# Performance work log

Hardware: AMD Instinct MI355X
Metric: run time of the kernel (lower is better)

## Reference

```python
import jax, jax.numpy as jnp
import numpy as np

N_QUBITS = 8
N_LAYERS = 7


def setup_inputs() -> dict:
    key = jax.random.key(0)
    ks = jax.random.split(key, 6)
    B = 65536
    return {
        "x": jax.random.normal(ks[0], (B, 2 ** N_QUBITS), dtype=jnp.float32),
        "weights": jax.random.normal(ks[1], (N_LAYERS, N_QUBITS), dtype=jnp.float32),
        "W1": jax.random.normal(ks[2], (16, 1), dtype=jnp.float32) * 0.5,
        "b1": jax.random.normal(ks[3], (16,), dtype=jnp.float32) * 0.1,
        "W2": jax.random.normal(ks[4], (1, 16), dtype=jnp.float32) * 0.5,
        "b2": jax.random.normal(ks[5], (1,), dtype=jnp.float32) * 0.1,
    }


def _apply_ry(psi, q, theta):
    # RY(theta) = [[cos(t/2), -sin(t/2)], [sin(t/2), cos(t/2)]] on wire q (axis q+1)
    c = jnp.cos(theta * 0.5)
    s = jnp.sin(theta * 0.5)
    a = jnp.take(psi, 0, axis=q + 1)
    b = jnp.take(psi, 1, axis=q + 1)
    return jnp.stack([c * a - s * b, s * a + c * b], axis=q + 1)


def _apply_cnot(psi, q):
    # CNOT control=q, target=q+1: flip target amplitudes where control=1
    ctl0 = jnp.take(psi, 0, axis=q + 1)
    ctl1 = jnp.take(psi, 1, axis=q + 1)
    # after removing axis q+1, target wire q+1 sits at axis q+1 of the slice
    ctl1 = jnp.flip(ctl1, axis=q + 1)
    return jnp.stack([ctl0, ctl1], axis=q + 1)


def _circuit(x, weights):
    B = x.shape[0]
    # AmplitudeEmbedding(normalize=True): real input -> real state (RY, CNOT are real)
    psi = x / jnp.linalg.norm(x, axis=1, keepdims=True)
    psi = psi.reshape((B,) + (2,) * N_QUBITS)  # axis 1 == wire 0 (MSB)
    for l in range(N_LAYERS):
        for q in range(N_QUBITS):
            psi = _apply_ry(psi, q, weights[l, q])
        for q in range(N_QUBITS - 1):
            psi = _apply_cnot(psi, q)
    probs = (psi ** 2).reshape(B, 2, -1)
    # <PauliZ(0)> = P(wire0=0) - P(wire0=1)
    return jnp.sum(probs[:, 0] - probs[:, 1], axis=1)


def reference(x, weights, W1, b1, W2, b2):
    z = _circuit(x, weights)[:, None]          # [B, 1]
    h = jax.nn.relu(z @ W1.T + b1)             # [B, 16]
    return jax.nn.sigmoid(h @ W2.T + b2)       # [B, 1]
```

## Files before the change

### kernel.cpp

```cpp
#include <hip/hip_runtime.h>
#include <hip/hip_bf16.h>

typedef __attribute__((ext_vector_type(8))) short bf16x8;
typedef __attribute__((ext_vector_type(4))) float f32x4;

__device__ __forceinline__ unsigned short f2bf(float f) {
    unsigned u = __builtin_bit_cast(unsigned, f);
    unsigned rnd = 0x7FFFu + ((u >> 16) & 1u);
    return (unsigned short)((u + rnd) >> 16);
}

__device__ __forceinline__ void wg_barrier() {
    asm volatile("s_waitcnt lgkmcnt(0)" ::: "memory");
    __builtin_amdgcn_sched_barrier(0);
    __builtin_amdgcn_s_barrier();
    __builtin_amdgcn_sched_barrier(0);
}

__global__ __launch_bounds__(256) void qnn_setup(const float* __restrict__ wts,
                                                 unsigned short* __restrict__ Bp) {
    __shared__ float cs[56], sn[56];
    int tid = threadIdx.x;
    if (tid < 56) {
        float th = 0.5f * wts[tid];
        cs[tid] = cosf(th);
        sn[tid] = sinf(th);
    }
    __syncthreads();

    int l = tid & 63;
    int k = blockIdx.x * 4 + (tid >> 6);
    int a0 = l << 2;

    float v0 = (float)(a0 + 0 == k);
    float v1 = (float)(a0 + 1 == k);
    float v2 = (float)(a0 + 2 == k);
    float v3 = (float)(a0 + 3 == k);

#pragma unroll
    for (int L = 0; L < 7; ++L) {
#pragma unroll
        for (int q = 0; q <= 5; ++q) {
            int m = 5 - q;
            float c = cs[L * 8 + q], s = sn[L * 8 + q];
            float ss = ((l >> m) & 1) ? s : -s;
            float p0 = __shfl_xor(v0, 1 << m);
            float p1 = __shfl_xor(v1, 1 << m);
            float p2 = __shfl_xor(v2, 1 << m);
            float p3 = __shfl_xor(v3, 1 << m);
            v0 = fmaf(ss, p0, c * v0);
            v1 = fmaf(ss, p1, c * v1);
            v2 = fmaf(ss, p2, c * v2);
            v3 = fmaf(ss, p3, c * v3);
        }
        {
            float c = cs[L * 8 + 6], s = sn[L * 8 + 6];
            float n0 = fmaf(-s, v2, c * v0), n2 = fmaf(s, v0, c * v2);
            float n1 = fmaf(-s, v3, c * v1), n3 = fmaf(s, v1, c * v3);
            v0 = n0; v1 = n1; v2 = n2; v3 = n3;
        }
        {
            float c = cs[L * 8 + 7], s = sn[L * 8 + 7];
            float n0 = fmaf(-s, v1, c * v0), n1 = fmaf(s, v0, c * v1);
            float n2 = fmaf(-s, v3, c * v2), n3 = fmaf(s, v2, c * v3);
            v0 = n0; v1 = n1; v2 = n2; v3 = n3;
        }
        {
            int src = l;
#pragma unroll
            for (int q = 4; q >= 0; --q)
                src = src ^ (((src >> (5 - q)) & 1) << (4 - q));
            v0 = __shfl(v0, src);
            v1 = __shfl(v1, src);
            v2 = __shfl(v2, src);
            v3 = __shfl(v3, src);
        }
        {
            bool cc = (l & 1);
            float n0 = cc ? v2 : v0, n2 = cc ? v0 : v2;
            float n1 = cc ? v3 : v1, n3 = cc ? v1 : v3;
            v0 = n0; v1 = n1; v2 = n2; v3 = n3;
        }
        {
            float t = v2; v2 = v3; v3 = t;
        }
    }

    int t = k >> 5, j = k & 7, lk = (k >> 3) & 3;
#pragma unroll
    for (int r = 0; r < 4; ++r) {
        int n = a0 + r;
        int u = n >> 4;
        int ls = lk * 16 + (n & 15);
        float val = (r == 0) ? v0 : (r == 1) ? v1 : (r == 2) ? v2 : v3;
        Bp[(((u * 8 + t) * 64) + ls) * 8 + j] = f2bf(val);
    }
}

__device__ __forceinline__ void cvt_store(const float4& a, const float4& b,
                                          unsigned short (*Xp)[256],
                                          int sr, int qt) {
    bf16x8 h;
    h[0] = (short)f2bf(a.x); h[1] = (short)f2bf(a.y);
    h[2] = (short)f2bf(a.z); h[3] = (short)f2bf(a.w);
    h[4] = (short)f2bf(b.x); h[5] = (short)f2bf(b.y);
    h[6] = (short)f2bf(b.z); h[7] = (short)f2bf(b.w);
    *(bf16x8*)&Xp[sr][(qt ^ (sr & 7)) * 8] = h;
}

__global__ __launch_bounds__(512, 4) void qnn_main(
    const float* __restrict__ x, const unsigned short* __restrict__ Bp,
    const float* __restrict__ W1, const float* __restrict__ b1,
    const float* __restrict__ W2, const float* __restrict__ b2,
    float* __restrict__ out) {
    __shared__ __align__(16) unsigned short Xs[2][16][256];
    __shared__ float Qpart[8][128];

    int tid = threadIdx.x;
    int l = tid & 63, w = tid >> 6;
    int sr = tid >> 5, qt = tid & 31;
    size_t base = (size_t)blockIdx.x * 128 * 256;
    const float* xst = x + base + (size_t)sr * 256 + qt * 8;

    const unsigned short* up = Bp + (size_t)(2 * w) * 4096 + l * 8;
    bf16x8 uf0[8], uf1[8];
#pragma unroll
    for (int t = 0; t < 8; ++t) {
        uf0[t] = *(const bf16x8*)(up + t * 512);
        uf1[t] = *(const bf16x8*)(up + 4096 + t * 512);
    }

    float4 pf[2][2];
    pf[0][0] = *(const float4*)(xst);
    pf[0][1] = *(const float4*)(xst + 4);
    pf[1][0] = *(const float4*)(xst + 4096);
    pf[1][1] = *(const float4*)(xst + 4100);
    cvt_store(pf[0][0], pf[0][1], Xs[0], sr, qt);
    wg_barrier();

    int row = l & 15, kg = l >> 4;

#pragma unroll
    for (int t = 0; t < 8; ++t) {
        if (t + 2 < 8) {
            pf[t & 1][0] = *(const float4*)(xst + (size_t)(t + 2) * 4096);
            pf[t & 1][1] = *(const float4*)(xst + (size_t)(t + 2) * 4096 + 4);
        }
        {
            const unsigned short* rp = &Xs[t & 1][row][0];
            f32x4 a0 = {0.f, 0.f, 0.f, 0.f}, a1 = {0.f, 0.f, 0.f, 0.f};
#pragma unroll
            for (int ks = 0; ks < 8; ++ks) {
                bf16x8 xf = *(const bf16x8*)(rp + (((ks << 2) | kg) ^ (row & 7)) * 8);
                a0 = __builtin_amdgcn_mfma_f32_16x16x32_bf16(uf0[ks], xf, a0, 0, 0, 0);
                a1 = __builtin_amdgcn_mfma_f32_16x16x32_bf16(uf1[ks], xf, a1, 0, 0, 0);
            }
            float q = 0.f;
#pragma unroll
            for (int j = 0; j < 4; ++j)
                q = fmaf(a0[j], a0[j], fmaf(a1[j], a1[j], q));
            q += __shfl_xor(q, 16);
            q += __shfl_xor(q, 32);
            if (l < 16) Qpart[w][t * 16 + l] = q;
        }
        if (t + 1 < 8)
            cvt_store(pf[(t + 1) & 1][0], pf[(t + 1) & 1][1],
                      Xs[(t + 1) & 1], sr, qt);
        wg_barrier();
    }

    if (tid < 128) {
        float pp = Qpart[0][tid] + Qpart[1][tid] + Qpart[2][tid] + Qpart[3][tid];
        float pm = Qpart[4][tid] + Qpart[5][tid] + Qpart[6][tid] + Qpart[7][tid];
        float z = (pp - pm) / (pp + pm);
        float o = b2[0];
#pragma unroll
        for (int jj = 0; jj < 16; ++jj) {
            float h = fmaf(z, W1[jj], b1[jj]);
            h = h > 0.f ? h : 0.f;
            o = fmaf(W2[jj], h, o);
        }
        out[(size_t)blockIdx.x * 128 + tid] = 1.f / (1.f + expf(-o));
    }
}

extern "C" void kernel_launch(void* const* d_in, const int* in_sizes, int n_in,
                              void* d_out, int out_size, void* d_ws, size_t ws_size,
                              hipStream_t stream) {
    const float* x   = (const float*)d_in[0];
    const float* wts = (const float*)d_in[1];
    const float* W1  = (const float*)d_in[2];
    const float* b1  = (const float*)d_in[3];
    const float* W2  = (const float*)d_in[4];
    const float* b2  = (const float*)d_in[5];
    float* out = (float*)d_out;
    unsigned short* Bp = (unsigned short*)d_ws;

    int B = in_sizes[0] >> 8;
    qnn_setup<<<64, 256, 0, stream>>>(wts, Bp);
    qnn_main<<<B / 128, 512, 0, stream>>>(x, Bp, W1, b1, W2, b2, out);
}
```

Baseline: 22.94 us.

## Process 32-row stages with wider per-thread loads and MFMA priority boost

The staged pipeline now handles 32 rows of x per stage instead of 16, halving the number of barrier-separated iterations. Each thread loads 16 floats (four float4) per stage, and each wave runs two 16-row MFMA groups per stage. s_setprio is raised around the MFMA section so compute waves get issue priority over the conversion and store work. The trade-off is double the LDS tile size and more prefetch registers per thread, which may reduce occupancy under the launch bound of 4.

```diff
diff --git a/kernel.cpp b/kernel.cpp
--- a/kernel.cpp
+++ b/kernel.cpp
@@ -97,15 +97,20 @@
     }
 }
 
-__device__ __forceinline__ void cvt_store(const float4& a, const float4& b,
+__device__ __forceinline__ void cvt_store(const float4* pf,
                                           unsigned short (*Xp)[256],
                                           int sr, int qt) {
-    bf16x8 h;
-    h[0] = (short)f2bf(a.x); h[1] = (short)f2bf(a.y);
-    h[2] = (short)f2bf(a.z); h[3] = (short)f2bf(a.w);
-    h[4] = (short)f2bf(b.x); h[5] = (short)f2bf(b.y);
-    h[6] = (short)f2bf(b.z); h[7] = (short)f2bf(b.w);
-    *(bf16x8*)&Xp[sr][(qt ^ (sr & 7)) * 8] = h;
+#pragma unroll
+    for (int h2 = 0; h2 < 2; ++h2) {
+        float4 a = pf[2 * h2], b = pf[2 * h2 + 1];
+        bf16x8 h;
+        h[0] = (short)f2bf(a.x); h[1] = (short)f2bf(a.y);
+        h[2] = (short)f2bf(a.z); h[3] = (short)f2bf(a.w);
+        h[4] = (short)f2bf(b.x); h[5] = (short)f2bf(b.y);
+        h[6] = (short)f2bf(b.z); h[7] = (short)f2bf(b.w);
+        int chunk = qt * 2 + h2;
+        *(bf16x8*)&Xp[sr][(chunk ^ (sr & 7)) * 8] = h;
+    }
 }
 
 __global__ __launch_bounds__(512, 4) void qnn_main(
@@ -113,14 +118,14 @@
     const float* __restrict__ W1, const float* __restrict__ b1,
     const float* __restrict__ W2, const float* __restrict__ b2,
     float* __restrict__ out) {
-    __shared__ __align__(16) unsigned short Xs[2][16][256];
+    __shared__ __align__(16) unsigned short Xs[2][32][256];
     __shared__ float Qpart[8][128];
 
     int tid = threadIdx.x;
     int l = tid & 63, w = tid >> 6;
-    int sr = tid >> 5, qt = tid & 31;
+    int sr = tid >> 4, qt = tid & 15;
     size_t base = (size_t)blockIdx.x * 128 * 256;
-    const float* xst = x + base + (size_t)sr * 256 + qt * 8;
+    const float* xst = x + base + (size_t)sr * 256 + qt * 16;
 
     const unsigned short* up = Bp + (size_t)(2 * w) * 4096 + l * 8;
     bf16x8 uf0[8], uf1[8];
@@ -130,28 +135,32 @@
         uf1[t] = *(const bf16x8*)(up + 4096 + t * 512);
     }
 
-    float4 pf[2][2];
-    pf[0][0] = *(const float4*)(xst);
-    pf[0][1] = *(const float4*)(xst + 4);
-    pf[1][0] = *(const float4*)(xst + 4096);
-    pf[1][1] = *(const float4*)(xst + 4100);
-    cvt_store(pf[0][0], pf[0][1], Xs[0], sr, qt);
+    float4 pf[2][4];
+#pragma unroll
+    for (int i = 0; i < 4; ++i) pf[0][i] = *(const float4*)(xst + 4 * i);
+#pragma unroll
+    for (int i = 0; i < 4; ++i) pf[1][i] = *(const float4*)(xst + 8192 + 4 * i);
+    cvt_store(pf[0], Xs[0], sr, qt);
     wg_barrier();
 
     int row = l & 15, kg = l >> 4;
 
 #pragma unroll
-    for (int t = 0; t < 8; ++t) {
-        if (t + 2 < 8) {
-            pf[t & 1][0] = *(const float4*)(xst + (size_t)(t + 2) * 4096);
-            pf[t & 1][1] = *(const float4*)(xst + (size_t)(t + 2) * 4096 + 4);
-        }
-        {
-            const unsigned short* rp = &Xs[t & 1][row][0];
+    for (int t = 0; t < 4; ++t) {
+        if (t + 2 < 4) {
+#pragma unroll
+            for (int i = 0; i < 4; ++i)
+                pf[t & 1][i] = *(const float4*)(xst + (size_t)(t + 2) * 8192 + 4 * i);
+        }
+        __builtin_amdgcn_s_setprio(1);
+#pragma unroll
+        for (int tau = 0; tau < 2; ++tau) {
+            const unsigned short* rp = &Xs[t & 1][tau * 16 + row][0];
+            int rsw = (tau * 16 + row) & 7;
             f32x4 a0 = {0.f, 0.f, 0.f, 0.f}, a1 = {0.f, 0.f, 0.f, 0.f};
 #pragma unroll
             for (int ks = 0; ks < 8; ++ks) {
-                bf16x8 xf = *(const bf16x8*)(rp + (((ks << 2) | kg) ^ (row & 7)) * 8);
+                bf16x8 xf = *(const bf16x8*)(rp + (((ks << 2) | kg) ^ rsw) * 8);
                 a0 = __builtin_amdgcn_mfma_f32_16x16x32_bf16(uf0[ks], xf, a0, 0, 0, 0);
                 a1 = __builtin_amdgcn_mfma_f32_16x16x32_bf16(uf1[ks], xf, a1, 0, 0, 0);
             }
@@ -161,11 +170,11 @@
                 q = fmaf(a0[j], a0[j], fmaf(a1[j], a1[j], q));
             q += __shfl_xor(q, 16);
             q += __shfl_xor(q, 32);
-            if (l < 16) Qpart[w][t * 16 + l] = q;
-        }
-        if (t + 1 < 8)
-            cvt_store(pf[(t + 1) & 1][0], pf[(t + 1) & 1][1],
-                      Xs[(t + 1) & 1], sr, qt);
+            if (l < 16) Qpart[w][t * 32 + tau * 16 + l] = q;
+        }
+        __builtin_amdgcn_s_setprio(0);
+        if (t + 1 < 4)
+            cvt_store(pf[(t + 1) & 1], Xs[(t + 1) & 1], sr, qt);
         wg_barrier();
     }
 
```

Result: slower. 26.81 us (+16.9%).
